# Kernel optimization log

Hardware: AMD Instinct MI355X
Metric: run time of the kernel (lower is better)

The kernel has to match this reference:

```python
import jax, jax.numpy as jnp
import numpy as np

B, C_IN, C_OUT, H, W = 2, 64, 32, 80, 80


def conv1x1(x, w, b):
    # x: [B, Cin, H, W], w: [Cout, Cin], b: [Cout]
    return jnp.einsum('bchw,oc->bohw', x, w) + b[None, :, None, None]


def setup_inputs() -> dict:
    key = jax.random.key(0)
    ks = jax.random.split(key, 5)
    scale = 0.02  # keep dot products moderate since exp() is unscaled (no max-subtract)
    return {
        'input_x': jax.random.normal(ks[0], (B, C_IN, H, W), dtype=jnp.float32),
        'w_g': jax.random.normal(ks[1], (C_OUT, C_IN), dtype=jnp.float32) * scale,
        'b_g': jnp.zeros((C_OUT,), dtype=jnp.float32),
        'w_phi': jax.random.normal(ks[2], (C_OUT, C_IN), dtype=jnp.float32) * scale,
        'b_phi': jnp.zeros((C_OUT,), dtype=jnp.float32),
        'w_theta': jax.random.normal(ks[3], (C_OUT, C_IN), dtype=jnp.float32) * scale,
        'b_theta': jnp.zeros((C_OUT,), dtype=jnp.float32),
        'w_y': jax.random.normal(ks[4], (C_IN, C_OUT), dtype=jnp.float32) * scale,
        'b_y': jnp.zeros((C_IN,), dtype=jnp.float32),
    }


def reference(input_x, w_g, b_g, w_phi, b_phi, w_theta, b_theta, w_y, b_y):
    batch = input_x.shape[0]
    g = conv1x1(input_x, w_g, b_g)          # [B, Cout, H, W]
    phi = conv1x1(input_x, w_phi, b_phi)    # [B, Cout, H, W]
    theta = conv1x1(input_x, w_theta, b_theta)
    # Faithful to torch: raw reshape (row-major reinterpretation), NOT a transpose
    g_x = g.reshape(batch, -1, C_OUT)        # [B, HW, Cout]
    theta_x = theta.reshape(batch, -1, C_OUT)
    phi_x = phi.reshape(batch, -1, C_OUT)
    f = jnp.einsum('bnc,bmc->bnm', theta_x, phi_x)  # [B, HW, HW]
    # nltype=0: unscaled exp / row-sum normalization (no max subtraction, faithful)
    f = jnp.exp(f)
    f_softmax = f / jnp.sum(f, axis=-1, keepdims=True)
    y = jnp.einsum('bnm,bmc->bnc', f_softmax, g_x)  # [B, HW, Cout]
    y = y.reshape(batch, C_OUT, H, W)
    z = conv1x1(y, w_y, b_y)                 # [B, Cin, H, W]
    return z
```

## Files before the change

### kernel.cpp

```cpp
#include <hip/hip_runtime.h>
#include <hip/hip_bf16.h>

#define BATCH 2
#define CIN   64
#define COUT  32
#define HW    6400
#define PB    (COUT*HW)
#define XB    (CIN*HW)
#define KSPLIT 5
#define LOG2E 1.4426950408889634f

typedef __attribute__((ext_vector_type(8))) short  bf16x8;
typedef __attribute__((ext_vector_type(4))) float  f32x4;

typedef unsigned short ushort;
typedef unsigned int   uint;

__device__ inline uint pk2(float a, float b) {
  __hip_bfloat162 h = __float22bfloat162_rn(make_float2(a, b));
  union { __hip_bfloat162 h2; uint u; } cv; cv.h2 = h;
  return cv.u;
}
__device__ inline float up_lo(uint u) { return __uint_as_float(u << 16); }

#define MFMA16(a, bop, c) __builtin_amdgcn_mfma_f32_16x16x32_bf16((a), (bop), (c), 0, 0, 0)

__global__ __launch_bounds__(128) void conv3_kernel(
    const float* __restrict__ x,
    const float* __restrict__ w0, const float* __restrict__ bb0,
    const float* __restrict__ w1, const float* __restrict__ bb1,
    const float* __restrict__ w2, const float* __restrict__ bb2,
    ushort* __restrict__ T_hi, ushort* __restrict__ T_lo,
    ushort* __restrict__ P_hi, ushort* __restrict__ G_hi) {
  const int which = blockIdx.y >> 1;
  const int oh    = blockIdx.y & 1;
  const float* w  = (which == 0) ? w0 : (which == 1) ? w1 : w2;
  const float* bv = (which == 0) ? bb0 : (which == 1) ? bb1 : bb2;
  ushort* ohi = (which == 0) ? T_hi : (which == 1) ? P_hi : G_hi;
  const int b = blockIdx.z;
  const int s = blockIdx.x * 128 + threadIdx.x;

  __shared__ float wsm[16 * CIN];
  for (int i = threadIdx.x; i < 16 * CIN; i += 128)
    wsm[i] = w[oh * 16 * CIN + i];
  __syncthreads();

  float xr[CIN];
#pragma unroll
  for (int c = 0; c < CIN; ++c) xr[c] = x[b * XB + c * HW + s];

  for (int oi = 0; oi < 16; ++oi) {
    const int o = oh * 16 + oi;
    const float4* wr = (const float4*)&wsm[oi * CIN];
    float acc = 0.f;
#pragma unroll
    for (int q = 0; q < CIN / 4; ++q) {
      float4 wv = wr[q];
      acc += wv.x * xr[4*q] + wv.y * xr[4*q+1] + wv.z * xr[4*q+2] + wv.w * xr[4*q+3];
    }
    acc += bv[o];
    if (which == 0) acc *= LOG2E;
    const int f = b * PB + o * HW + s;
    uint hb = pk2(acc, 0.f) & 0xFFFFu;
    ohi[f] = (ushort)hb;
    if (which == 0) {
      float hf = up_lo(hb);
      T_lo[f] = (ushort)(pk2(acc - hf, 0.f) & 0xFFFFu);
    }
  }
}

__global__ __launch_bounds__(256) void transpose_g_kernel(
    const ushort* __restrict__ G_hi, ushort* __restrict__ Gt_hi) {
  const int b  = blockIdx.y;
  const int n0 = blockIdx.x * 32;
  const int t  = threadIdx.x;

  __shared__ ushort tile[1024];

  const int rbase = b * PB + n0 * 32;
  if (t < 256) ((uint2*)tile)[t] = ((const uint2*)(G_hi + rbase))[t];
  __syncthreads();

  const int c  = t >> 3;
  const int p0 = (t & 7) * 4;
  ushort4 vh;
  {
    int p, sp;
    p = p0 + 0; sp = 4*(p>>3) + (p&3) + 16*((p>>2)&1); vh.x = tile[sp*32 + c];
    p = p0 + 1; sp = 4*(p>>3) + (p&3) + 16*((p>>2)&1); vh.y = tile[sp*32 + c];
    p = p0 + 2; sp = 4*(p>>3) + (p&3) + 16*((p>>2)&1); vh.z = tile[sp*32 + c];
    p = p0 + 3; sp = 4*(p>>3) + (p&3) + 16*((p>>2)&1); vh.w = tile[sp*32 + c];
  }
  *(ushort4*)(Gt_hi + b * PB + c * HW + n0 + p0) = vh;
}

__global__ __launch_bounds__(256, 3) void attn_kernel(
    const ushort* __restrict__ T_hi, const ushort* __restrict__ T_lo,
    const ushort* __restrict__ P_hi, const ushort* __restrict__ Gt_hi,
    float* __restrict__ Yp,
    float* __restrict__ Dp) {
  const int b     = blockIdx.z;
  const int ks    = blockIdx.y;
  const int q_blk = blockIdx.x;
  const int tid   = threadIdx.x;
  const int w     = tid >> 6;
  const int lane  = tid & 63;
  const int l15   = lane & 15;
  const int g     = lane >> 4;

  __shared__ float yl[4 * 32 * 33 + 4 * 32];

  const int niter = 10;
  const int kbase = ks * 1280 + w * 32;

  bf16x8 t_hi[4], t_lo[4];
#pragma unroll
  for (int s2 = 0; s2 < 4; ++s2) {
    const int qrow = q_blk * 64 + s2 * 16 + l15;
    t_hi[s2] = *(const bf16x8*)&T_hi[b * PB + qrow * 32 + g * 8];
    t_lo[s2] = *(const bf16x8*)&T_lo[b * PB + qrow * 32 + g * 8];
  }

  const ushort* pg = P_hi + b * PB + (kbase + l15) * 32 + g * 8;
  const ushort* gg = Gt_hi + b * PB + l15 * HW + kbase + g * 8;

  f32x4 acc0[4] = {{0,0,0,0},{0,0,0,0},{0,0,0,0},{0,0,0,0}};
  f32x4 acc1[4] = {{0,0,0,0},{0,0,0,0},{0,0,0,0},{0,0,0,0}};
  float denom[4] = {0.f, 0.f, 0.f, 0.f};

  bf16x8 pa = *(const bf16x8*)pg;
  bf16x8 pb = *(const bf16x8*)(pg + 512);
  bf16x8 g0 = *(const bf16x8*)gg;
  bf16x8 g1 = *(const bf16x8*)(gg + 16 * HW);

  for (int i = 0; i < niter; ++i) {
    bf16x8 pan, pbn, g0n, g1n;
    if (i + 1 < niter) {
      const ushort* pgn = pg + (i + 1) * 4096;
      const ushort* ggn = gg + (i + 1) * 128;
      pan = *(const bf16x8*)pgn;
      pbn = *(const bf16x8*)(pgn + 512);
      g0n = *(const bf16x8*)ggn;
      g1n = *(const bf16x8*)(ggn + 16 * HW);
    }

#pragma unroll
    for (int s2 = 0; s2 < 4; ++s2) {
      f32x4 sa = {0.f,0.f,0.f,0.f};
      f32x4 sb = {0.f,0.f,0.f,0.f};
      __builtin_amdgcn_s_setprio(1);
      sa = MFMA16(pa, t_hi[s2], sa);
      sa = MFMA16(pa, t_lo[s2], sa);
      sb = MFMA16(pb, t_hi[s2], sb);
      sb = MFMA16(pb, t_lo[s2], sb);
      __builtin_amdgcn_s_setprio(0);

      const float ea0 = __builtin_amdgcn_exp2f(sa[0]);
      const float ea1 = __builtin_amdgcn_exp2f(sa[1]);
      const float ea2 = __builtin_amdgcn_exp2f(sa[2]);
      const float ea3 = __builtin_amdgcn_exp2f(sa[3]);
      const float eb0 = __builtin_amdgcn_exp2f(sb[0]);
      const float eb1 = __builtin_amdgcn_exp2f(sb[1]);
      const float eb2 = __builtin_amdgcn_exp2f(sb[2]);
      const float eb3 = __builtin_amdgcn_exp2f(sb[3]);
      denom[s2] += ((ea0 + ea1) + (ea2 + ea3)) + ((eb0 + eb1) + (eb2 + eb3));

      union { uint u[4]; bf16x8 v; } ph;
      ph.u[0] = pk2(ea0, ea1); ph.u[1] = pk2(ea2, ea3);
      ph.u[2] = pk2(eb0, eb1); ph.u[3] = pk2(eb2, eb3);

      __builtin_amdgcn_s_setprio(1);
      acc0[s2] = MFMA16(ph.v, g0, acc0[s2]);
      acc1[s2] = MFMA16(ph.v, g1, acc1[s2]);
      __builtin_amdgcn_s_setprio(0);
    }

    if (i + 1 < niter) { pa = pan; pb = pbn; g0 = g0n; g1 = g1n; }
  }

  float* dl = yl + 4 * 32 * 33;
  const int c  = tid & 31;
  const int q0 = tid >> 5;

#pragma unroll
  for (int p = 0; p < 2; ++p) {
    __syncthreads();
#pragma unroll
    for (int sl = 0; sl < 2; ++sl) {
      const int s2 = p * 2 + sl;
      float dn = denom[s2];
      dn += __shfl_xor(dn, 16);
      dn += __shfl_xor(dn, 32);
#pragma unroll
      for (int r = 0; r < 4; ++r) {
        yl[(w * 32 + sl * 16 + 4 * g + r) * 33 + l15]      = acc0[s2][r];
        yl[(w * 32 + sl * 16 + 4 * g + r) * 33 + 16 + l15] = acc1[s2][r];
      }
      if (g == 0) dl[w * 32 + sl * 16 + l15] = dn;
    }
    __syncthreads();

#pragma unroll
    for (int rr = 0; rr < 4; ++rr) {
      const int row = rr * 8 + q0;
      float y = 0.f, d = 0.f;
#pragma unroll
      for (int k2 = 0; k2 < 4; ++k2) {
        y += yl[(k2 * 32 + row) * 33 + c];
        d += dl[k2 * 32 + row];
      }
      const int qrow = q_blk * 64 + p * 32 + row;
      Yp[((size_t)(ks * BATCH + b)) * PB + qrow * 32 + c] = y;
      if (c == 0) Dp[((size_t)(ks * BATCH + b)) * HW + qrow] = d;
    }
  }
}

__global__ __launch_bounds__(128) void conv_out_kernel(
    const float* __restrict__ Yp, const float* __restrict__ Dp,
    const float* __restrict__ wy, const float* __restrict__ by,
    float* __restrict__ z) {
  const int b  = blockIdx.z;
  const int ih = blockIdx.y;
  const int s  = blockIdx.x * 128 + threadIdx.x;

  __shared__ float wsm[32 * COUT];
  for (int i = threadIdx.x; i < 32 * COUT; i += 128)
    wsm[i] = wy[ih * 32 * COUT + i];
  __syncthreads();

  float yr[COUT];
#pragma unroll
  for (int o = 0; o < COUT; ++o) {
    const int f = o * HW + s;
    const int n = f >> 5;
    float y = 0.f, d = 0.f;
#pragma unroll
    for (int ksi = 0; ksi < KSPLIT; ++ksi) {
      y += Yp[((size_t)(ksi * BATCH + b)) * PB + f];
      d += Dp[((size_t)(ksi * BATCH + b)) * HW + n];
    }
    yr[o] = y / d;
  }

  for (int ii = 0; ii < 32; ++ii) {
    const int i = ih * 32 + ii;
    const float4* wr = (const float4*)&wsm[ii * COUT];
    float acc = 0.f;
#pragma unroll
    for (int q = 0; q < COUT / 4; ++q) {
      float4 wv = wr[q];
      acc += wv.x * yr[4*q] + wv.y * yr[4*q+1] + wv.z * yr[4*q+2] + wv.w * yr[4*q+3];
    }
    z[(size_t)b * XB + i * HW + s] = acc + by[i];
  }
}

extern "C" void kernel_launch(void* const* d_in, const int* in_sizes, int n_in,
                              void* d_out, int out_size, void* d_ws, size_t ws_size,
                              hipStream_t stream) {
  const float* x       = (const float*)d_in[0];
  const float* w_g     = (const float*)d_in[1];
  const float* b_g     = (const float*)d_in[2];
  const float* w_phi   = (const float*)d_in[3];
  const float* b_phi   = (const float*)d_in[4];
  const float* w_theta = (const float*)d_in[5];
  const float* b_theta = (const float*)d_in[6];
  const float* w_y     = (const float*)d_in[7];
  const float* b_y     = (const float*)d_in[8];
  float* z = (float*)d_out;

  char* base = (char*)d_ws;
  const size_t BF = (size_t)BATCH * PB * sizeof(ushort);
  ushort* T_hi  = (ushort*)(base);
  ushort* T_lo  = (ushort*)(base + 1 * BF);
  ushort* P_hi  = (ushort*)(base + 2 * BF);
  ushort* G_hi  = (ushort*)(base + 3 * BF);
  ushort* Gt_hi = (ushort*)(base + 4 * BF);
  float*  Yp    = (float*)(base + 5 * BF);
  float*  Dp    = (float*)(base + 5 * BF +
                           (size_t)KSPLIT * BATCH * PB * sizeof(float));

  conv3_kernel<<<dim3(50, 6, BATCH), 128, 0, stream>>>(
      x, w_theta, b_theta, w_phi, b_phi, w_g, b_g,
      T_hi, T_lo, P_hi, G_hi);
  transpose_g_kernel<<<dim3(200, BATCH), 256, 0, stream>>>(G_hi, Gt_hi);
  attn_kernel<<<dim3(100, KSPLIT, BATCH), 256, 0, stream>>>(
      T_hi, T_lo, P_hi, Gt_hi, Yp, Dp);
  conv_out_kernel<<<dim3(50, 2, BATCH), 128, 0, stream>>>(Yp, Dp, w_y, b_y, z);
}
```

Baseline: 59.23 us.

## Fuse G transpose into conv kernel and fully unroll attention K loop

The conv kernel now writes the g projection straight into the transposed, permuted layout the attention kernel consumes, so the separate transpose kernel launch and its intermediate buffer go away. The attention main loop is also fully unrolled with direct per-iteration loads in place of the manual register double-buffering, leaving load scheduling to the compiler. The fused store is a scattered 2-byte write with poor coalescing, and the unrolling may raise register pressure at 3 waves per SIMD.

```diff
diff --git a/kernel.cpp b/kernel.cpp
--- a/kernel.cpp
+++ b/kernel.cpp
@@ -31,12 +31,11 @@
     const float* __restrict__ w1, const float* __restrict__ bb1,
     const float* __restrict__ w2, const float* __restrict__ bb2,
     ushort* __restrict__ T_hi, ushort* __restrict__ T_lo,
-    ushort* __restrict__ P_hi, ushort* __restrict__ G_hi) {
+    ushort* __restrict__ P_hi, ushort* __restrict__ Gt_hi) {
   const int which = blockIdx.y >> 1;
   const int oh    = blockIdx.y & 1;
   const float* w  = (which == 0) ? w0 : (which == 1) ? w1 : w2;
   const float* bv = (which == 0) ? bb0 : (which == 1) ? bb1 : bb2;
-  ushort* ohi = (which == 0) ? T_hi : (which == 1) ? P_hi : G_hi;
   const int b = blockIdx.z;
   const int s = blockIdx.x * 128 + threadIdx.x;
 
@@ -60,39 +59,23 @@
     }
     acc += bv[o];
     if (which == 0) acc *= LOG2E;
-    const int f = b * PB + o * HW + s;
     uint hb = pk2(acc, 0.f) & 0xFFFFu;
-    ohi[f] = (ushort)hb;
-    if (which == 0) {
-      float hf = up_lo(hb);
-      T_lo[f] = (ushort)(pk2(acc - hf, 0.f) & 0xFFFFu);
-    }
-  }
-}
-
-__global__ __launch_bounds__(256) void transpose_g_kernel(
-    const ushort* __restrict__ G_hi, ushort* __restrict__ Gt_hi) {
-  const int b  = blockIdx.y;
-  const int n0 = blockIdx.x * 32;
-  const int t  = threadIdx.x;
-
-  __shared__ ushort tile[1024];
-
-  const int rbase = b * PB + n0 * 32;
-  if (t < 256) ((uint2*)tile)[t] = ((const uint2*)(G_hi + rbase))[t];
-  __syncthreads();
-
-  const int c  = t >> 3;
-  const int p0 = (t & 7) * 4;
-  ushort4 vh;
-  {
-    int p, sp;
-    p = p0 + 0; sp = 4*(p>>3) + (p&3) + 16*((p>>2)&1); vh.x = tile[sp*32 + c];
-    p = p0 + 1; sp = 4*(p>>3) + (p&3) + 16*((p>>2)&1); vh.y = tile[sp*32 + c];
-    p = p0 + 2; sp = 4*(p>>3) + (p&3) + 16*((p>>2)&1); vh.z = tile[sp*32 + c];
-    p = p0 + 3; sp = 4*(p>>3) + (p&3) + 16*((p>>2)&1); vh.w = tile[sp*32 + c];
-  }
-  *(ushort4*)(Gt_hi + b * PB + c * HW + n0 + p0) = vh;
+    if (which == 2) {
+      const int m  = o * 200 + (s >> 5);
+      const int np = (m & ~31) + 16*((m>>3)&1) + 8*((m>>2)&1)
+                   + 4*((m>>4)&1) + (m & 3);
+      Gt_hi[b * PB + (s & 31) * HW + np] = (ushort)hb;
+    } else {
+      const int f = b * PB + o * HW + s;
+      if (which == 0) {
+        T_hi[f] = (ushort)hb;
+        float hf = up_lo(hb);
+        T_lo[f] = (ushort)(pk2(acc - hf, 0.f) & 0xFFFFu);
+      } else {
+        P_hi[f] = (ushort)hb;
+      }
+    }
+  }
 }
 
 __global__ __launch_bounds__(256, 3) void attn_kernel(
@@ -111,7 +94,6 @@
 
   __shared__ float yl[4 * 32 * 33 + 4 * 32];
 
-  const int niter = 10;
   const int kbase = ks * 1280 + w * 32;
 
   bf16x8 t_hi[4], t_lo[4];
@@ -129,21 +111,14 @@
   f32x4 acc1[4] = {{0,0,0,0},{0,0,0,0},{0,0,0,0},{0,0,0,0}};
   float denom[4] = {0.f, 0.f, 0.f, 0.f};
 
-  bf16x8 pa = *(const bf16x8*)pg;
-  bf16x8 pb = *(const bf16x8*)(pg + 512);
-  bf16x8 g0 = *(const bf16x8*)gg;
-  bf16x8 g1 = *(const bf16x8*)(gg + 16 * HW);
-
-  for (int i = 0; i < niter; ++i) {
-    bf16x8 pan, pbn, g0n, g1n;
-    if (i + 1 < niter) {
-      const ushort* pgn = pg + (i + 1) * 4096;
-      const ushort* ggn = gg + (i + 1) * 128;
-      pan = *(const bf16x8*)pgn;
-      pbn = *(const bf16x8*)(pgn + 512);
-      g0n = *(const bf16x8*)ggn;
-      g1n = *(const bf16x8*)(ggn + 16 * HW);
-    }
+#pragma unroll
+  for (int i = 0; i < 10; ++i) {
+    const ushort* pgi = pg + i * 4096;
+    const ushort* ggi = gg + i * 128;
+    const bf16x8 pa = *(const bf16x8*)pgi;
+    const bf16x8 pb = *(const bf16x8*)(pgi + 512);
+    const bf16x8 g0 = *(const bf16x8*)ggi;
+    const bf16x8 g1 = *(const bf16x8*)(ggi + 16 * HW);
 
 #pragma unroll
     for (int s2 = 0; s2 < 4; ++s2) {
@@ -175,8 +150,6 @@
       acc1[s2] = MFMA16(ph.v, g1, acc1[s2]);
       __builtin_amdgcn_s_setprio(0);
     }
-
-    if (i + 1 < niter) { pa = pan; pb = pbn; g0 = g0n; g1 = g1n; }
   }
 
   float* dl = yl + 4 * 32 * 33;
@@ -276,16 +249,14 @@
   ushort* T_hi  = (ushort*)(base);
   ushort* T_lo  = (ushort*)(base + 1 * BF);
   ushort* P_hi  = (ushort*)(base + 2 * BF);
-  ushort* G_hi  = (ushort*)(base + 3 * BF);
-  ushort* Gt_hi = (ushort*)(base + 4 * BF);
-  float*  Yp    = (float*)(base + 5 * BF);
-  float*  Dp    = (float*)(base + 5 * BF +
+  ushort* Gt_hi = (ushort*)(base + 3 * BF);
+  float*  Yp    = (float*)(base + 4 * BF);
+  float*  Dp    = (float*)(base + 4 * BF +
                            (size_t)KSPLIT * BATCH * PB * sizeof(float));
 
   conv3_kernel<<<dim3(50, 6, BATCH), 128, 0, stream>>>(
       x, w_theta, b_theta, w_phi, b_phi, w_g, b_g,
-      T_hi, T_lo, P_hi, G_hi);
-  transpose_g_kernel<<<dim3(200, BATCH), 256, 0, stream>>>(G_hi, Gt_hi);
+      T_hi, T_lo, P_hi, Gt_hi);
   attn_kernel<<<dim3(100, KSPLIT, BATCH), 256, 0, stream>>>(
       T_hi, T_lo, P_hi, Gt_hi, Yp, Dp);
   conv_out_kernel<<<dim3(50, 2, BATCH), 128, 0, stream>>>(Yp, Dp, w_y, b_y, z);
```

New measurement: 105.1 us. +77.5%, slower.
